# Kernel optimization log

Measured on AMD Instinct MI355X. Metric: run time of the kernel, lower is better.

## Reference

```python
import jax, jax.numpy as jnp
import numpy as np

D_THRESH = 0.5  # init arg `dist`


def setup_inputs() -> dict:
    key = jax.random.key(0)
    k1, k2 = jax.random.split(key)
    N, M, C = 20000, 25000, 3
    pointcloud = jax.random.uniform(k1, (N, C), dtype=jnp.float32)
    pointcloud_padding = jax.random.uniform(k2, (M, C), dtype=jnp.float32)
    return {"pointcloud": pointcloud, "pointcloud_padding": pointcloud_padding}


def reference(pointcloud, pointcloud_padding):
    # torch.cdist(padding, pointcloud): Euclidean distance matrix [M, N]
    # via the GEMM formulation ||a||^2 + ||b||^2 - 2 a.b (matches torch's path)
    a2 = jnp.sum(pointcloud_padding * pointcloud_padding, axis=1)[:, None]  # [M,1]
    b2 = jnp.sum(pointcloud * pointcloud, axis=1)[None, :]                  # [1,N]
    ab = pointcloud_padding @ pointcloud.T                                  # [M,N]
    dist = jnp.sqrt(jnp.maximum(a2 + b2 - 2.0 * ab, 0.0))                   # [M,N]
    # count neighbors within radius, per pointcloud point
    counts = jnp.sum(dist <= D_THRESH, axis=0).astype(jnp.int32)            # [N]
    out = counts.reshape(-1, 1)[: pointcloud.shape[0]]                      # [N,1]
    return out
```

## Files before the change

kernel.cpp:

```cpp
#include <hip/hip_runtime.h>

typedef short  bf16x8 __attribute__((ext_vector_type(8)));

#define JS      13
#define STREAMS (JS * 4)
#define TI      128
#define DEPTH   2

__device__ __forceinline__ unsigned short f2bf(float x) {
    unsigned u = __builtin_bit_cast(unsigned, x);
    u += 0x7FFF + ((u >> 16) & 1);
    return (unsigned short)(u >> 16);
}
__device__ __forceinline__ float bf2f(unsigned short h) {
    unsigned u = ((unsigned)h) << 16;
    return __builtin_bit_cast(float, u);
}

__global__ __launch_bounds__(256) void dens_pack_kernel(
    const float* __restrict__ pad, uint4* __restrict__ ws,
    int* __restrict__ out, int M, int mtot, int N)
{
    const int j = blockIdx.x * 256 + threadIdx.x;
    if (j < N) out[j] = 0;
    if (j >= mtot) return;

    float qx = 0.f, qy = 0.f, qz = 0.f;
    float negc = -1.0e6f;
    if (j < M) {
        qx = pad[3 * j]; qy = pad[3 * j + 1]; qz = pad[3 * j + 2];
        negc = 0.125f - 0.5f * (qx * qx + qy * qy + qz * qz);
    }
    const unsigned short xh = f2bf(qx), yh = f2bf(qy), zh = f2bf(qz);
    const unsigned short xl = f2bf(qx - bf2f(xh));
    const unsigned short yl = f2bf(qy - bf2f(yh));
    const unsigned short zl = f2bf(qz - bf2f(zh));
    const unsigned short ch = f2bf(negc);
    const unsigned short cl = f2bf(negc - bf2f(ch));

    uint4 p0, p1;
    p0.x = (unsigned)xh | ((unsigned)yh << 16);
    p0.y = (unsigned)zh | ((unsigned)xl << 16);
    p0.z = (unsigned)yl | ((unsigned)zl << 16);
    p0.w = (unsigned)xh | ((unsigned)yh << 16);
    p1.x = (unsigned)zh | ((unsigned)xl << 16);
    p1.y = (unsigned)yl | ((unsigned)zl << 16);
    p1.z = (unsigned)ch | ((unsigned)cl << 16);
    p1.w = 0x3F803F80u;
    ws[j]        = p0;
    ws[mtot + j] = p1;
}

__device__ __forceinline__ void make_bfrag(const float* __restrict__ pc,
                                           int i, int N, int half, bf16x8& B)
{
    float px = 0.f, py = 0.f, pz = 0.f;
    float ha = 3.0e38f;
    if (i < N) {
        px = pc[3 * i]; py = pc[3 * i + 1]; pz = pc[3 * i + 2];
        ha = 0.5f * (px * px + py * py + pz * pz);
    }
    const float nha = -ha;
    const unsigned short nhh = f2bf(nha);
    const unsigned short nhl = f2bf(nha - bf2f(nhh));
    const short xh = (short)f2bf(px), yh = (short)f2bf(py), zh = (short)f2bf(pz);
    const short xl = (short)f2bf(px - bf2f((unsigned short)xh));
    const short yl = (short)f2bf(py - bf2f((unsigned short)yh));
    const short zl = (short)f2bf(pz - bf2f((unsigned short)zh));
    const short ONE = (short)0x3F80;
    const bf16x8 Blo = {xh, yh, zh, xh, yh, zh, xl, yl};
    const bf16x8 Bhi = {zl, xl, yl, zl, ONE, ONE, (short)nhh, (short)nhl};
    B = half ? Bhi : Blo;
}

#define CONS(R0,R1,R2,R3,R4,R5,R6,R7,R8,R9,RA,RB,RC,RD,RE,RF, CA, CB) \
    "v_ashrrev_i32 " R0 ", 31, " R0 "\n\t" \
    "v_ashrrev_i32 " R1 ", 31, " R1 "\n\t" \
    "v_ashrrev_i32 " R2 ", 31, " R2 "\n\t" \
    "v_ashrrev_i32 " R3 ", 31, " R3 "\n\t" \
    "v_ashrrev_i32 " R4 ", 31, " R4 "\n\t" \
    "v_ashrrev_i32 " R5 ", 31, " R5 "\n\t" \
    "v_ashrrev_i32 " R6 ", 31, " R6 "\n\t" \
    "v_ashrrev_i32 " R7 ", 31, " R7 "\n\t" \
    "v_ashrrev_i32 " R8 ", 31, " R8 "\n\t" \
    "v_ashrrev_i32 " R9 ", 31, " R9 "\n\t" \
    "v_ashrrev_i32 " RA ", 31, " RA "\n\t" \
    "v_ashrrev_i32 " RB ", 31, " RB "\n\t" \
    "v_ashrrev_i32 " RC ", 31, " RC "\n\t" \
    "v_ashrrev_i32 " RD ", 31, " RD "\n\t" \
    "v_ashrrev_i32 " RE ", 31, " RE "\n\t" \
    "v_ashrrev_i32 " RF ", 31, " RF "\n\t" \
    "v_add3_u32 " CA ", " R0 ", " R1 ", " CA "\n\t" \
    "v_add3_u32 " CB ", " R2 ", " R3 ", " CB "\n\t" \
    "v_add3_u32 " CA ", " R4 ", " R5 ", " CA "\n\t" \
    "v_add3_u32 " CB ", " R6 ", " R7 ", " CB "\n\t" \
    "v_add3_u32 " CA ", " R8 ", " R9 ", " CA "\n\t" \
    "v_add3_u32 " CB ", " RA ", " RB ", " CB "\n\t" \
    "v_add3_u32 " CA ", " RC ", " RD ", " CA "\n\t" \
    "v_add3_u32 " CB ", " RE ", " RF ", " CB "\n\t"

#define CONS_D0(CA, CB) \
    CONS("v32","v33","v34","v35","v36","v37","v38","v39", \
         "v40","v41","v42","v43","v44","v45","v46","v47", CA, CB)
#define CONS_D1(CA, CB) \
    CONS("v48","v49","v50","v51","v52","v53","v54","v55", \
         "v56","v57","v58","v59","v60","v61","v62","v63", CA, CB)

#define VISIT(AR) \
    "s_waitcnt vmcnt(1)\n\t" \
    "v_mfma_f32_32x32x16_bf16 v[32:47], " AR ", %9,  v[64:79]\n\t" \
    "v_mfma_f32_32x32x16_bf16 v[48:63], " AR ", %10, v[64:79]\n\t" \
    "s_nop 7\n\t" \
    "s_nop 2\n\t" \
    CONS_D0("%0", "%1") \
    "v_mfma_f32_32x32x16_bf16 v[32:47], " AR ", %11, v[64:79]\n\t" \
    CONS_D1("%2", "%3") \
    "v_mfma_f32_32x32x16_bf16 v[48:63], " AR ", %12, v[64:79]\n\t" \
    "global_load_dwordx4 " AR ", v[88:89], off\n\t" \
    "v_add_co_u32 v88, vcc, 0x6800, v88\n\t" \
    "v_addc_co_u32 v89, vcc, 0, v89, vcc\n\t" \
    CONS_D0("%4", "%5") \
    CONS_D1("%6", "%7")

__global__ __launch_bounds__(256, 4) void dens_mfma_kernel(
    const float* __restrict__ pc,
    const char*  __restrict__ wsA,
    int* __restrict__ out,
    int N, int iters, int p1off, int visits)
{
    const int lane = threadIdx.x & 63;
    const int w    = threadIdx.x >> 6;
    const int n    = lane & 31;
    const int half = lane >> 5;

    const int ibase = blockIdx.x * TI;
    bf16x8 B0, B1, B2, B3;
    make_bfrag(pc, ibase + n,      N, half, B0);
    make_bfrag(pc, ibase + 32 + n, N, half, B1);
    make_bfrag(pc, ibase + 64 + n, N, half, B2);
    make_bfrag(pc, ibase + 96 + n, N, half, B3);

    const int stream = blockIdx.y * 4 + w;
    const unsigned long long ax =
        (unsigned long long)(wsA + (half ? p1off : 0) + n * 16 + (size_t)stream * 512);
    const unsigned xlo = (unsigned)ax, xhi = (unsigned)(ax >> 32);

    int it = iters;
    int c0a = 0, c0b = 0, c1a = 0, c1b = 0, c2a = 0, c2b = 0, c3a = 0, c3b = 0;

    asm volatile(
        "v_mov_b32 v88, %13\n\t"
        "v_mov_b32 v89, %14\n\t"
        "v_mov_b32 v64, 0\n\t" "v_mov_b32 v65, 0\n\t"
        "v_mov_b32 v66, 0\n\t" "v_mov_b32 v67, 0\n\t"
        "v_mov_b32 v68, 0\n\t" "v_mov_b32 v69, 0\n\t"
        "v_mov_b32 v70, 0\n\t" "v_mov_b32 v71, 0\n\t"
        "v_mov_b32 v72, 0\n\t" "v_mov_b32 v73, 0\n\t"
        "v_mov_b32 v74, 0\n\t" "v_mov_b32 v75, 0\n\t"
        "v_mov_b32 v76, 0\n\t" "v_mov_b32 v77, 0\n\t"
        "v_mov_b32 v78, 0\n\t" "v_mov_b32 v79, 0\n\t"
        "global_load_dwordx4 v[80:83], v[88:89], off\n\t"
        "v_add_co_u32 v88, vcc, 0x6800, v88\n\t"
        "v_addc_co_u32 v89, vcc, 0, v89, vcc\n\t"
        "global_load_dwordx4 v[84:87], v[88:89], off\n\t"
        "v_add_co_u32 v88, vcc, 0x6800, v88\n\t"
        "v_addc_co_u32 v89, vcc, 0, v89, vcc\n\t"
        "Ldens%=:\n\t"
        VISIT("v[80:83]")
        VISIT("v[84:87]")
        "s_sub_u32 %8, %8, 1\n\t"
        "s_cmp_lg_u32 %8, 0\n\t"
        "s_cbranch_scc1 Ldens%=\n\t"
        : "+v"(c0a), "+v"(c0b), "+v"(c1a), "+v"(c1b),
          "+v"(c2a), "+v"(c2b), "+v"(c3a), "+v"(c3b), "+s"(it)
        : "v"(B0), "v"(B1), "v"(B2), "v"(B3), "v"(xlo), "v"(xhi)
        : "vcc", "scc", "memory",
          "v32","v33","v34","v35","v36","v37","v38","v39",
          "v40","v41","v42","v43","v44","v45","v46","v47",
          "v48","v49","v50","v51","v52","v53","v54","v55",
          "v56","v57","v58","v59","v60","v61","v62","v63",
          "v64","v65","v66","v67","v68","v69","v70","v71",
          "v72","v73","v74","v75","v76","v77","v78","v79",
          "v80","v81","v82","v83","v84","v85","v86","v87",
          "v88","v89");

    const int base = 32 * visits;
    int t0 = c0a + c0b;  t0 += __shfl_xor(t0, 32);
    int t1 = c1a + c1b;  t1 += __shfl_xor(t1, 32);
    int t2 = c2a + c2b;  t2 += __shfl_xor(t2, 32);
    int t3 = c3a + c3b;  t3 += __shfl_xor(t3, 32);

    __shared__ int red[4][TI];
    if (lane < 32) {
        red[w][n]      = base + t0;
        red[w][n + 32] = base + t1;
        red[w][n + 64] = base + t2;
        red[w][n + 96] = base + t3;
    }
    __syncthreads();
    if (threadIdx.x < TI) {
        const int ii = ibase + threadIdx.x;
        if (ii < N) {
            const int s = red[0][threadIdx.x] + red[1][threadIdx.x] +
                          red[2][threadIdx.x] + red[3][threadIdx.x];
            atomicAdd(&out[ii], s);
        }
    }
}

extern "C" void kernel_launch(void* const* d_in, const int* in_sizes, int n_in,
                              void* d_out, int out_size, void* d_ws, size_t ws_size,
                              hipStream_t stream) {
    const float* pc  = (const float*)d_in[0];
    const float* pad = (const float*)d_in[1];
    int* out = (int*)d_out;

    const int N = in_sizes[0] / 3;
    const int M = in_sizes[1] / 3;
    const int jt = (M + 31) / 32;
    int visits = (jt + STREAMS - 1) / STREAMS;
    if (visits & 1) visits++;
    const int jtp  = (visits + DEPTH) * STREAMS;
    const int mtot = jtp * 32;

    dens_pack_kernel<<<(mtot + 255) / 256, 256, 0, stream>>>(
        pad, (uint4*)d_ws, out, M, mtot, N);

    dim3 grid((N + TI - 1) / TI, JS);
    dens_mfma_kernel<<<grid, 256, 0, stream>>>(
        pc, (const char*)d_ws, out, N, visits / 2, mtot * 16, visits);
}
```

Measured before the change: 85.93 us.

## Offload neighbor-count accumulation from VALU adds to int8 MFMA reductions

Replaces the per-element v_add3 accumulation of sign masks with int8 MFMA instructions that multiply the sign-mask bytes by per-lane-group selector vectors, so the counting is done on the matrix unit instead of the vector ALU. The sign-extended results are reinterpreted as packed bytes and accumulated into a 32x32 int32 accumulator, then decoded after the loop with shifts and scattered into shared memory. This aims to relieve the VALU bottleneck in the inner loop but adds 16 extra MFMAs per visit, more accumulator registers, and relies on subtle byte-packing semantics that risk correctness errors.

```diff
diff --git a/kernel.cpp b/kernel.cpp
--- a/kernel.cpp
+++ b/kernel.cpp
@@ -1,6 +1,7 @@
 #include <hip/hip_runtime.h>
 
-typedef short  bf16x8 __attribute__((ext_vector_type(8)));
+typedef short  bf16x8  __attribute__((ext_vector_type(8)));
+typedef int    int32x4 __attribute__((ext_vector_type(4)));
 
 #define JS      13
 #define STREAMS (JS * 4)
@@ -73,54 +74,54 @@
     B = half ? Bhi : Blo;
 }
 
-#define CONS(R0,R1,R2,R3,R4,R5,R6,R7,R8,R9,RA,RB,RC,RD,RE,RF, CA, CB) \
-    "v_ashrrev_i32 " R0 ", 31, " R0 "\n\t" \
-    "v_ashrrev_i32 " R1 ", 31, " R1 "\n\t" \
-    "v_ashrrev_i32 " R2 ", 31, " R2 "\n\t" \
-    "v_ashrrev_i32 " R3 ", 31, " R3 "\n\t" \
-    "v_ashrrev_i32 " R4 ", 31, " R4 "\n\t" \
-    "v_ashrrev_i32 " R5 ", 31, " R5 "\n\t" \
-    "v_ashrrev_i32 " R6 ", 31, " R6 "\n\t" \
-    "v_ashrrev_i32 " R7 ", 31, " R7 "\n\t" \
-    "v_ashrrev_i32 " R8 ", 31, " R8 "\n\t" \
-    "v_ashrrev_i32 " R9 ", 31, " R9 "\n\t" \
-    "v_ashrrev_i32 " RA ", 31, " RA "\n\t" \
-    "v_ashrrev_i32 " RB ", 31, " RB "\n\t" \
-    "v_ashrrev_i32 " RC ", 31, " RC "\n\t" \
-    "v_ashrrev_i32 " RD ", 31, " RD "\n\t" \
-    "v_ashrrev_i32 " RE ", 31, " RE "\n\t" \
-    "v_ashrrev_i32 " RF ", 31, " RF "\n\t" \
-    "v_add3_u32 " CA ", " R0 ", " R1 ", " CA "\n\t" \
-    "v_add3_u32 " CB ", " R2 ", " R3 ", " CB "\n\t" \
-    "v_add3_u32 " CA ", " R4 ", " R5 ", " CA "\n\t" \
-    "v_add3_u32 " CB ", " R6 ", " R7 ", " CB "\n\t" \
-    "v_add3_u32 " CA ", " R8 ", " R9 ", " CA "\n\t" \
-    "v_add3_u32 " CB ", " RA ", " RB ", " CB "\n\t" \
-    "v_add3_u32 " CA ", " RC ", " RD ", " CA "\n\t" \
-    "v_add3_u32 " CB ", " RE ", " RF ", " CB "\n\t"
-
-#define CONS_D0(CA, CB) \
-    CONS("v32","v33","v34","v35","v36","v37","v38","v39", \
-         "v40","v41","v42","v43","v44","v45","v46","v47", CA, CB)
-#define CONS_D1(CA, CB) \
-    CONS("v48","v49","v50","v51","v52","v53","v54","v55", \
-         "v56","v57","v58","v59","v60","v61","v62","v63", CA, CB)
+#define SGN_D0 \
+    "v_ashrrev_i32 v32, 31, v32\n\t" "v_ashrrev_i32 v33, 31, v33\n\t" \
+    "v_ashrrev_i32 v34, 31, v34\n\t" "v_ashrrev_i32 v35, 31, v35\n\t" \
+    "v_ashrrev_i32 v36, 31, v36\n\t" "v_ashrrev_i32 v37, 31, v37\n\t" \
+    "v_ashrrev_i32 v38, 31, v38\n\t" "v_ashrrev_i32 v39, 31, v39\n\t" \
+    "v_ashrrev_i32 v40, 31, v40\n\t" "v_ashrrev_i32 v41, 31, v41\n\t" \
+    "v_ashrrev_i32 v42, 31, v42\n\t" "v_ashrrev_i32 v43, 31, v43\n\t" \
+    "v_ashrrev_i32 v44, 31, v44\n\t" "v_ashrrev_i32 v45, 31, v45\n\t" \
+    "v_ashrrev_i32 v46, 31, v46\n\t" "v_ashrrev_i32 v47, 31, v47\n\t"
+#define SGN_D1 \
+    "v_ashrrev_i32 v48, 31, v48\n\t" "v_ashrrev_i32 v49, 31, v49\n\t" \
+    "v_ashrrev_i32 v50, 31, v50\n\t" "v_ashrrev_i32 v51, 31, v51\n\t" \
+    "v_ashrrev_i32 v52, 31, v52\n\t" "v_ashrrev_i32 v53, 31, v53\n\t" \
+    "v_ashrrev_i32 v54, 31, v54\n\t" "v_ashrrev_i32 v55, 31, v55\n\t" \
+    "v_ashrrev_i32 v56, 31, v56\n\t" "v_ashrrev_i32 v57, 31, v57\n\t" \
+    "v_ashrrev_i32 v58, 31, v58\n\t" "v_ashrrev_i32 v59, 31, v59\n\t" \
+    "v_ashrrev_i32 v60, 31, v60\n\t" "v_ashrrev_i32 v61, 31, v61\n\t" \
+    "v_ashrrev_i32 v62, 31, v62\n\t" "v_ashrrev_i32 v63, 31, v63\n\t"
+
+#define RED_D0(BR) \
+    "v_mfma_i32_32x32x32_i8 v[96:111], v[32:35], " BR ", v[96:111]\n\t" \
+    "v_mfma_i32_32x32x32_i8 v[96:111], v[36:39], " BR ", v[96:111]\n\t" \
+    "v_mfma_i32_32x32x32_i8 v[96:111], v[40:43], " BR ", v[96:111]\n\t" \
+    "v_mfma_i32_32x32x32_i8 v[96:111], v[44:47], " BR ", v[96:111]\n\t"
+#define RED_D1(BR) \
+    "v_mfma_i32_32x32x32_i8 v[96:111], v[48:51], " BR ", v[96:111]\n\t" \
+    "v_mfma_i32_32x32x32_i8 v[96:111], v[52:55], " BR ", v[96:111]\n\t" \
+    "v_mfma_i32_32x32x32_i8 v[96:111], v[56:59], " BR ", v[96:111]\n\t" \
+    "v_mfma_i32_32x32x32_i8 v[96:111], v[60:63], " BR ", v[96:111]\n\t"
 
 #define VISIT(AR) \
     "s_waitcnt vmcnt(1)\n\t" \
-    "v_mfma_f32_32x32x16_bf16 v[32:47], " AR ", %9,  v[64:79]\n\t" \
-    "v_mfma_f32_32x32x16_bf16 v[48:63], " AR ", %10, v[64:79]\n\t" \
-    "s_nop 7\n\t" \
-    "s_nop 2\n\t" \
-    CONS_D0("%0", "%1") \
-    "v_mfma_f32_32x32x16_bf16 v[32:47], " AR ", %11, v[64:79]\n\t" \
-    CONS_D1("%2", "%3") \
-    "v_mfma_f32_32x32x16_bf16 v[48:63], " AR ", %12, v[64:79]\n\t" \
-    "global_load_dwordx4 " AR ", v[88:89], off\n\t" \
+    "v_mfma_f32_32x32x16_bf16 v[32:47], " AR ", %[B0], v[64:79]\n\t" \
+    "v_mfma_f32_32x32x16_bf16 v[48:63], " AR ", %[B1], v[64:79]\n\t" \
     "v_add_co_u32 v88, vcc, 0x6800, v88\n\t" \
     "v_addc_co_u32 v89, vcc, 0, v89, vcc\n\t" \
-    CONS_D0("%4", "%5") \
-    CONS_D1("%6", "%7")
+    "s_nop 4\n\t" \
+    SGN_D0 \
+    RED_D0("%[R0]") \
+    "v_mfma_f32_32x32x16_bf16 v[32:47], " AR ", %[B2], v[64:79]\n\t" \
+    SGN_D1 \
+    RED_D1("%[R1]") \
+    "v_mfma_f32_32x32x16_bf16 v[48:63], " AR ", %[B3], v[64:79]\n\t" \
+    "global_load_dwordx4 " AR ", v[88:89], off\n\t" \
+    SGN_D0 \
+    RED_D0("%[R2]") \
+    SGN_D1 \
+    RED_D1("%[R3]")
 
 __global__ __launch_bounds__(256, 4) void dens_mfma_kernel(
     const float* __restrict__ pc,
@@ -140,17 +141,27 @@
     make_bfrag(pc, ibase + 64 + n, N, half, B2);
     make_bfrag(pc, ibase + 96 + n, N, half, B3);
 
+    const int gsel = n >> 3;
+    const int m0 = (gsel == 0) ? 0x01010101 : 0;
+    const int m1 = (gsel == 1) ? 0x01010101 : 0;
+    const int m2 = (gsel == 2) ? 0x01010101 : 0;
+    const int m3 = (gsel == 3) ? 0x01010101 : 0;
+    const int32x4 R0 = {m0, m0, m0, m0};
+    const int32x4 R1 = {m1, m1, m1, m1};
+    const int32x4 R2 = {m2, m2, m2, m2};
+    const int32x4 R3 = {m3, m3, m3, m3};
+
     const int stream = blockIdx.y * 4 + w;
     const unsigned long long ax =
         (unsigned long long)(wsA + (half ? p1off : 0) + n * 16 + (size_t)stream * 512);
     const unsigned xlo = (unsigned)ax, xhi = (unsigned)(ax >> 32);
 
     int it = iters;
-    int c0a = 0, c0b = 0, c1a = 0, c1b = 0, c2a = 0, c2b = 0, c3a = 0, c3b = 0;
+    int a0, a1, a2, a3, a4, a5, a6, a7, a8, a9, a10, a11, a12, a13, a14, a15;
 
     asm volatile(
-        "v_mov_b32 v88, %13\n\t"
-        "v_mov_b32 v89, %14\n\t"
+        "v_mov_b32 v88, %[xlo]\n\t"
+        "v_mov_b32 v89, %[xhi]\n\t"
         "v_mov_b32 v64, 0\n\t" "v_mov_b32 v65, 0\n\t"
         "v_mov_b32 v66, 0\n\t" "v_mov_b32 v67, 0\n\t"
         "v_mov_b32 v68, 0\n\t" "v_mov_b32 v69, 0\n\t"
@@ -159,21 +170,41 @@
         "v_mov_b32 v74, 0\n\t" "v_mov_b32 v75, 0\n\t"
         "v_mov_b32 v76, 0\n\t" "v_mov_b32 v77, 0\n\t"
         "v_mov_b32 v78, 0\n\t" "v_mov_b32 v79, 0\n\t"
+        "v_mov_b32 v96, 0\n\t"  "v_mov_b32 v97, 0\n\t"
+        "v_mov_b32 v98, 0\n\t"  "v_mov_b32 v99, 0\n\t"
+        "v_mov_b32 v100, 0\n\t" "v_mov_b32 v101, 0\n\t"
+        "v_mov_b32 v102, 0\n\t" "v_mov_b32 v103, 0\n\t"
+        "v_mov_b32 v104, 0\n\t" "v_mov_b32 v105, 0\n\t"
+        "v_mov_b32 v106, 0\n\t" "v_mov_b32 v107, 0\n\t"
+        "v_mov_b32 v108, 0\n\t" "v_mov_b32 v109, 0\n\t"
+        "v_mov_b32 v110, 0\n\t" "v_mov_b32 v111, 0\n\t"
         "global_load_dwordx4 v[80:83], v[88:89], off\n\t"
         "v_add_co_u32 v88, vcc, 0x6800, v88\n\t"
         "v_addc_co_u32 v89, vcc, 0, v89, vcc\n\t"
         "global_load_dwordx4 v[84:87], v[88:89], off\n\t"
-        "v_add_co_u32 v88, vcc, 0x6800, v88\n\t"
-        "v_addc_co_u32 v89, vcc, 0, v89, vcc\n\t"
         "Ldens%=:\n\t"
         VISIT("v[80:83]")
         VISIT("v[84:87]")
-        "s_sub_u32 %8, %8, 1\n\t"
-        "s_cmp_lg_u32 %8, 0\n\t"
+        "s_sub_u32 %[it], %[it], 1\n\t"
+        "s_cmp_lg_u32 %[it], 0\n\t"
         "s_cbranch_scc1 Ldens%=\n\t"
-        : "+v"(c0a), "+v"(c0b), "+v"(c1a), "+v"(c1b),
-          "+v"(c2a), "+v"(c2b), "+v"(c3a), "+v"(c3b), "+s"(it)
-        : "v"(B0), "v"(B1), "v"(B2), "v"(B3), "v"(xlo), "v"(xhi)
+        "s_nop 7\n\t" "s_nop 7\n\t" "s_nop 7\n\t"
+        "v_mov_b32 %[a0],  v96\n\t"  "v_mov_b32 %[a1],  v97\n\t"
+        "v_mov_b32 %[a2],  v98\n\t"  "v_mov_b32 %[a3],  v99\n\t"
+        "v_mov_b32 %[a4],  v100\n\t" "v_mov_b32 %[a5],  v101\n\t"
+        "v_mov_b32 %[a6],  v102\n\t" "v_mov_b32 %[a7],  v103\n\t"
+        "v_mov_b32 %[a8],  v104\n\t" "v_mov_b32 %[a9],  v105\n\t"
+        "v_mov_b32 %[a10], v106\n\t" "v_mov_b32 %[a11], v107\n\t"
+        "v_mov_b32 %[a12], v108\n\t" "v_mov_b32 %[a13], v109\n\t"
+        "v_mov_b32 %[a14], v110\n\t" "v_mov_b32 %[a15], v111\n\t"
+        : [a0]"=v"(a0),   [a1]"=v"(a1),   [a2]"=v"(a2),   [a3]"=v"(a3),
+          [a4]"=v"(a4),   [a5]"=v"(a5),   [a6]"=v"(a6),   [a7]"=v"(a7),
+          [a8]"=v"(a8),   [a9]"=v"(a9),   [a10]"=v"(a10), [a11]"=v"(a11),
+          [a12]"=v"(a12), [a13]"=v"(a13), [a14]"=v"(a14), [a15]"=v"(a15),
+          [it]"+s"(it)
+        : [B0]"v"(B0), [B1]"v"(B1), [B2]"v"(B2), [B3]"v"(B3),
+          [R0]"v"(R0), [R1]"v"(R1), [R2]"v"(R2), [R3]"v"(R3),
+          [xlo]"v"(xlo), [xhi]"v"(xhi)
         : "vcc", "scc", "memory",
           "v32","v33","v34","v35","v36","v37","v38","v39",
           "v40","v41","v42","v43","v44","v45","v46","v47",
@@ -182,20 +213,32 @@
           "v64","v65","v66","v67","v68","v69","v70","v71",
           "v72","v73","v74","v75","v76","v77","v78","v79",
           "v80","v81","v82","v83","v84","v85","v86","v87",
-          "v88","v89");
+          "v88","v89",
+          "v96","v97","v98","v99","v100","v101","v102","v103",
+          "v104","v105","v106","v107","v108","v109","v110","v111");
 
     const int base = 32 * visits;
-    int t0 = c0a + c0b;  t0 += __shfl_xor(t0, 32);
-    int t1 = c1a + c1b;  t1 += __shfl_xor(t1, 32);
-    int t2 = c2a + c2b;  t2 += __shfl_xor(t2, 32);
-    int t3 = c3a + c3b;  t3 += __shfl_xor(t3, 32);
-
     __shared__ int red[4][TI];
-    if (lane < 32) {
-        red[w][n]      = base + t0;
-        red[w][n + 32] = base + t1;
-        red[w][n + 64] = base + t2;
-        red[w][n + 96] = base + t3;
+    if ((lane & 7) == 0) {
+        const int g   = n >> 3;
+        const int hi4 = half << 2;
+        int* rw = &red[w][32 * g];
+        rw[ 0 + hi4] = base + (a0  >> 2);
+        rw[ 1 + hi4] = base + (a1  >> 2);
+        rw[ 2 + hi4] = base + (a2  >> 2);
+        rw[ 3 + hi4] = base + (a3  >> 2);
+        rw[ 8 + hi4] = base + (a4  >> 2);
+        rw[ 9 + hi4] = base + (a5  >> 2);
+        rw[10 + hi4] = base + (a6  >> 2);
+        rw[11 + hi4] = base + (a7  >> 2);
+        rw[16 + hi4] = base + (a8  >> 2);
+        rw[17 + hi4] = base + (a9  >> 2);
+        rw[18 + hi4] = base + (a10 >> 2);
+        rw[19 + hi4] = base + (a11 >> 2);
+        rw[24 + hi4] = base + (a12 >> 2);
+        rw[25 + hi4] = base + (a13 >> 2);
+        rw[26 + hi4] = base + (a14 >> 2);
+        rw[27 + hi4] = base + (a15 >> 2);
     }
     __syncthreads();
     if (threadIdx.x < TI) {
```

Result: slower. 105.1 us (+22.3%).

## Offload sign-count reduction to int8 MFMA and replace inline asm with builtins

Applied to the files above, without the earlier changes.

Instead of reducing each distance-test result with VALU shifts and add3 instructions, the kernel packs the sign bytes of four MFMA outputs into one dword and accumulates counts with an i32 32x32x32 i8 MFMA against per-group one-hot masks. The hand-written asm loop is replaced by compiler builtins and plain loads, leaving scheduling and register allocation to the compiler. The aim is to shift the counting work off the vector ALU onto the matrix unit. In exchange there is extra perm/and work per element, a more involved final scatter of counts, and possible loss of the hand-tuned load/MFMA interleave.

```diff
diff --git a/kernel.cpp b/kernel.cpp
--- a/kernel.cpp
+++ b/kernel.cpp
@@ -1,6 +1,9 @@
 #include <hip/hip_runtime.h>
 
-typedef short  bf16x8 __attribute__((ext_vector_type(8)));
+typedef short  bf16x8   __attribute__((ext_vector_type(8)));
+typedef int    int32x4  __attribute__((ext_vector_type(4)));
+typedef int    int32x16 __attribute__((ext_vector_type(16)));
+typedef float  f32x16   __attribute__((ext_vector_type(16)));
 
 #define JS      13
 #define STREAMS (JS * 4)
@@ -73,54 +76,24 @@
     B = half ? Bhi : Blo;
 }
 
-#define CONS(R0,R1,R2,R3,R4,R5,R6,R7,R8,R9,RA,RB,RC,RD,RE,RF, CA, CB) \
-    "v_ashrrev_i32 " R0 ", 31, " R0 "\n\t" \
-    "v_ashrrev_i32 " R1 ", 31, " R1 "\n\t" \
-    "v_ashrrev_i32 " R2 ", 31, " R2 "\n\t" \
-    "v_ashrrev_i32 " R3 ", 31, " R3 "\n\t" \
-    "v_ashrrev_i32 " R4 ", 31, " R4 "\n\t" \
-    "v_ashrrev_i32 " R5 ", 31, " R5 "\n\t" \
-    "v_ashrrev_i32 " R6 ", 31, " R6 "\n\t" \
-    "v_ashrrev_i32 " R7 ", 31, " R7 "\n\t" \
-    "v_ashrrev_i32 " R8 ", 31, " R8 "\n\t" \
-    "v_ashrrev_i32 " R9 ", 31, " R9 "\n\t" \
-    "v_ashrrev_i32 " RA ", 31, " RA "\n\t" \
-    "v_ashrrev_i32 " RB ", 31, " RB "\n\t" \
-    "v_ashrrev_i32 " RC ", 31, " RC "\n\t" \
-    "v_ashrrev_i32 " RD ", 31, " RD "\n\t" \
-    "v_ashrrev_i32 " RE ", 31, " RE "\n\t" \
-    "v_ashrrev_i32 " RF ", 31, " RF "\n\t" \
-    "v_add3_u32 " CA ", " R0 ", " R1 ", " CA "\n\t" \
-    "v_add3_u32 " CB ", " R2 ", " R3 ", " CB "\n\t" \
-    "v_add3_u32 " CA ", " R4 ", " R5 ", " CA "\n\t" \
-    "v_add3_u32 " CB ", " R6 ", " R7 ", " CB "\n\t" \
-    "v_add3_u32 " CA ", " R8 ", " R9 ", " CA "\n\t" \
-    "v_add3_u32 " CB ", " RA ", " RB ", " CB "\n\t" \
-    "v_add3_u32 " CA ", " RC ", " RD ", " CA "\n\t" \
-    "v_add3_u32 " CB ", " RE ", " RF ", " CB "\n\t"
-
-#define CONS_D0(CA, CB) \
-    CONS("v32","v33","v34","v35","v36","v37","v38","v39", \
-         "v40","v41","v42","v43","v44","v45","v46","v47", CA, CB)
-#define CONS_D1(CA, CB) \
-    CONS("v48","v49","v50","v51","v52","v53","v54","v55", \
-         "v56","v57","v58","v59","v60","v61","v62","v63", CA, CB)
-
-#define VISIT(AR) \
-    "s_waitcnt vmcnt(1)\n\t" \
-    "v_mfma_f32_32x32x16_bf16 v[32:47], " AR ", %9,  v[64:79]\n\t" \
-    "v_mfma_f32_32x32x16_bf16 v[48:63], " AR ", %10, v[64:79]\n\t" \
-    "s_nop 7\n\t" \
-    "s_nop 2\n\t" \
-    CONS_D0("%0", "%1") \
-    "v_mfma_f32_32x32x16_bf16 v[32:47], " AR ", %11, v[64:79]\n\t" \
-    CONS_D1("%2", "%3") \
-    "v_mfma_f32_32x32x16_bf16 v[48:63], " AR ", %12, v[64:79]\n\t" \
-    "global_load_dwordx4 " AR ", v[88:89], off\n\t" \
-    "v_add_co_u32 v88, vcc, 0x6800, v88\n\t" \
-    "v_addc_co_u32 v89, vcc, 0, v89, vcc\n\t" \
-    CONS_D0("%4", "%5") \
-    CONS_D1("%6", "%7")
+__device__ __forceinline__ unsigned pack4(float f0, float f1, float f2, float f3) {
+    const unsigned u0 = __builtin_bit_cast(unsigned, f0);
+    const unsigned u1 = __builtin_bit_cast(unsigned, f1);
+    const unsigned u2 = __builtin_bit_cast(unsigned, f2);
+    const unsigned u3 = __builtin_bit_cast(unsigned, f3);
+    const unsigned lo = __builtin_amdgcn_perm(u0, u1, 0x0C0C0703u);
+    const unsigned hi = __builtin_amdgcn_perm(u2, u3, 0x07030C0Cu);
+    return (lo | hi) & 0x80808080u;
+}
+
+__device__ __forceinline__ int32x16 red_group(const f32x16 d, int32x4 m, int32x16 acc) {
+    int32x4 P;
+    P[0] = (int)pack4(d[0],  d[1],  d[2],  d[3]);
+    P[1] = (int)pack4(d[4],  d[5],  d[6],  d[7]);
+    P[2] = (int)pack4(d[8],  d[9],  d[10], d[11]);
+    P[3] = (int)pack4(d[12], d[13], d[14], d[15]);
+    return __builtin_amdgcn_mfma_i32_32x32x32_i8(P, m, acc, 0, 0, 0);
+}
 
 __global__ __launch_bounds__(256, 4) void dens_mfma_kernel(
     const float* __restrict__ pc,
@@ -140,62 +113,74 @@
     make_bfrag(pc, ibase + 64 + n, N, half, B2);
     make_bfrag(pc, ibase + 96 + n, N, half, B3);
 
+    const int gsel = n >> 3;
+    const int m0 = (gsel == 0) ? 0x01010101 : 0;
+    const int m1 = (gsel == 1) ? 0x01010101 : 0;
+    const int m2 = (gsel == 2) ? 0x01010101 : 0;
+    const int m3 = (gsel == 3) ? 0x01010101 : 0;
+    const int32x4 R0 = {m0, m0, m0, m0};
+    const int32x4 R1 = {m1, m1, m1, m1};
+    const int32x4 R2 = {m2, m2, m2, m2};
+    const int32x4 R3 = {m3, m3, m3, m3};
+
     const int stream = blockIdx.y * 4 + w;
-    const unsigned long long ax =
-        (unsigned long long)(wsA + (half ? p1off : 0) + n * 16 + (size_t)stream * 512);
-    const unsigned xlo = (unsigned)ax, xhi = (unsigned)(ax >> 32);
-
-    int it = iters;
-    int c0a = 0, c0b = 0, c1a = 0, c1b = 0, c2a = 0, c2b = 0, c3a = 0, c3b = 0;
-
-    asm volatile(
-        "v_mov_b32 v88, %13\n\t"
-        "v_mov_b32 v89, %14\n\t"
-        "v_mov_b32 v64, 0\n\t" "v_mov_b32 v65, 0\n\t"
-        "v_mov_b32 v66, 0\n\t" "v_mov_b32 v67, 0\n\t"
-        "v_mov_b32 v68, 0\n\t" "v_mov_b32 v69, 0\n\t"
-        "v_mov_b32 v70, 0\n\t" "v_mov_b32 v71, 0\n\t"
-        "v_mov_b32 v72, 0\n\t" "v_mov_b32 v73, 0\n\t"
-        "v_mov_b32 v74, 0\n\t" "v_mov_b32 v75, 0\n\t"
-        "v_mov_b32 v76, 0\n\t" "v_mov_b32 v77, 0\n\t"
-        "v_mov_b32 v78, 0\n\t" "v_mov_b32 v79, 0\n\t"
-        "global_load_dwordx4 v[80:83], v[88:89], off\n\t"
-        "v_add_co_u32 v88, vcc, 0x6800, v88\n\t"
-        "v_addc_co_u32 v89, vcc, 0, v89, vcc\n\t"
-        "global_load_dwordx4 v[84:87], v[88:89], off\n\t"
-        "v_add_co_u32 v88, vcc, 0x6800, v88\n\t"
-        "v_addc_co_u32 v89, vcc, 0, v89, vcc\n\t"
-        "Ldens%=:\n\t"
-        VISIT("v[80:83]")
-        VISIT("v[84:87]")
-        "s_sub_u32 %8, %8, 1\n\t"
-        "s_cmp_lg_u32 %8, 0\n\t"
-        "s_cbranch_scc1 Ldens%=\n\t"
-        : "+v"(c0a), "+v"(c0b), "+v"(c1a), "+v"(c1b),
-          "+v"(c2a), "+v"(c2b), "+v"(c3a), "+v"(c3b), "+s"(it)
-        : "v"(B0), "v"(B1), "v"(B2), "v"(B3), "v"(xlo), "v"(xhi)
-        : "vcc", "scc", "memory",
-          "v32","v33","v34","v35","v36","v37","v38","v39",
-          "v40","v41","v42","v43","v44","v45","v46","v47",
-          "v48","v49","v50","v51","v52","v53","v54","v55",
-          "v56","v57","v58","v59","v60","v61","v62","v63",
-          "v64","v65","v66","v67","v68","v69","v70","v71",
-          "v72","v73","v74","v75","v76","v77","v78","v79",
-          "v80","v81","v82","v83","v84","v85","v86","v87",
-          "v88","v89");
+    const uint4* __restrict__ ap = (const uint4*)
+        (wsA + (half ? p1off : 0) + n * 16 + (size_t)stream * 512);
+    const int T4 = 0x6800 / 16;
+
+    const f32x16  z   = {0.f};
+    int32x16      acc = {0};
+
+    uint4 X = ap[0];
+    uint4 Y = ap[T4];
+    int nextoff = 2 * T4;
+
+#define GROUPV(AV, BV, RV) { \
+        f32x16 d = __builtin_amdgcn_mfma_f32_32x32x16_bf16(AV, BV, z, 0, 0, 0); \
+        acc = red_group(d, RV, acc); }
+
+    for (int t = 0; t < iters; ++t) {
+        {
+            const bf16x8 a = __builtin_bit_cast(bf16x8, X);
+            GROUPV(a, B0, R0)
+            GROUPV(a, B1, R1)
+            GROUPV(a, B2, R2)
+            GROUPV(a, B3, R3)
+            X = ap[nextoff]; nextoff += T4;
+        }
+        {
+            const bf16x8 a = __builtin_bit_cast(bf16x8, Y);
+            GROUPV(a, B0, R0)
+            GROUPV(a, B1, R1)
+            GROUPV(a, B2, R2)
+            GROUPV(a, B3, R3)
+            Y = ap[nextoff]; nextoff += T4;
+        }
+    }
+#undef GROUPV
 
     const int base = 32 * visits;
-    int t0 = c0a + c0b;  t0 += __shfl_xor(t0, 32);
-    int t1 = c1a + c1b;  t1 += __shfl_xor(t1, 32);
-    int t2 = c2a + c2b;  t2 += __shfl_xor(t2, 32);
-    int t3 = c3a + c3b;  t3 += __shfl_xor(t3, 32);
-
     __shared__ int red[4][TI];
-    if (lane < 32) {
-        red[w][n]      = base + t0;
-        red[w][n + 32] = base + t1;
-        red[w][n + 64] = base + t2;
-        red[w][n + 96] = base + t3;
+    if ((lane & 7) == 0) {
+        const int g   = n >> 3;
+        const int hi4 = half << 2;
+        int* rw = &red[w][32 * g];
+        rw[ 0 + hi4] = base + (acc[0]  >> 7);
+        rw[ 1 + hi4] = base + (acc[1]  >> 7);
+        rw[ 2 + hi4] = base + (acc[2]  >> 7);
+        rw[ 3 + hi4] = base + (acc[3]  >> 7);
+        rw[ 8 + hi4] = base + (acc[4]  >> 7);
+        rw[ 9 + hi4] = base + (acc[5]  >> 7);
+        rw[10 + hi4] = base + (acc[6]  >> 7);
+        rw[11 + hi4] = base + (acc[7]  >> 7);
+        rw[16 + hi4] = base + (acc[8]  >> 7);
+        rw[17 + hi4] = base + (acc[9]  >> 7);
+        rw[18 + hi4] = base + (acc[10] >> 7);
+        rw[19 + hi4] = base + (acc[11] >> 7);
+        rw[24 + hi4] = base + (acc[12] >> 7);
+        rw[25 + hi4] = base + (acc[13] >> 7);
+        rw[26 + hi4] = base + (acc[14] >> 7);
+        rw[27 + hi4] = base + (acc[15] >> 7);
     }
     __syncthreads();
     if (threadIdx.x < TI) {
```

Result: faster. 82.27 us (median of 2 runs) (-4.3%).
